# Performance work log

Measured on AMD Instinct MI355X. Metric: run time of the kernel, lower is better.

## Reference

```python
import jax, jax.numpy as jnp
import numpy as np

NUM_LONGTERM_MEM = 16  # config.num_longterm_mem


def setup_inputs() -> dict:
    key = jax.random.key(0)
    ks = jax.random.split(key, 9)
    B, T, C, H = 32, 2048, 768, 1536
    s = 0.02
    return {
        "x": jax.random.normal(ks[0], (B, T, C), jnp.float32),
        "Wq": jax.random.normal(ks[1], (C, C), jnp.float32) * s,
        "bq": jax.random.normal(ks[2], (C,), jnp.float32) * s,
        "W0": jax.random.normal(ks[3], (B, H, C), jnp.float32) * s,
        "b0": jax.random.normal(ks[4], (B, H), jnp.float32) * s,
        "W1": jax.random.normal(ks[5], (B, C, H), jnp.float32) * s,
        "b1": jax.random.normal(ks[6], (B, C), jnp.float32) * s,
        "Wo": jax.random.normal(ks[7], (C, C), jnp.float32) * s,
        "bo": jax.random.normal(ks[8], (C,), jnp.float32) * s,
    }


def reference(x, Wq, bq, W0, b0, W1, b1, Wo, bo):
    # x: [B, T, C]. Per-sample memory MLP weights W0 [B,H,C], W1 [B,C,H].
    B, T, C = x.shape
    L = NUM_LONGTERM_MEM
    # query projection (nn.Linear: x @ W^T + b)
    q = jnp.einsum("btc,dc->btd", x, Wq) + bq                       # [B,T,C]
    # per-sample 2-layer memory MLP with SiLU
    h = jax.nn.silu(jnp.einsum("btc,bhc->bth", q, W0) + b0[:, None, :])  # [B,T,H]
    mem = jnp.einsum("bth,bch->btc", h, W1) + b1[:, None, :]        # [B,T,C]
    # adaptive_avg_pool1d over T -> L (T divisible by L => uniform window mean)
    pooled = mem.reshape(B, L, T // L, C).mean(axis=2)              # [B,L,C]
    # output projection
    return jnp.einsum("blc,dc->bld", pooled, Wo) + bo               # [B,L,C]
```

## Files before the change

kernel.cpp:

```cpp
#include <hip/hip_runtime.h>
#include <stdint.h>

#define B_ 32
#define T_ 2048
#define C_ 768
#define H_ 1536
#define L_ 16

typedef unsigned short u16;
typedef __bf16 bf16x8 __attribute__((ext_vector_type(8)));
typedef float f32x4 __attribute__((ext_vector_type(4)));

__device__ __forceinline__ u16 f2bf(float f) {
    union { float f; uint32_t u; } v; v.f = f;
    uint32_t r = (v.u + 0x7fffu + ((v.u >> 16) & 1u)) >> 16;
    return (u16)r;
}

__device__ __forceinline__ float wave_sum(float v) {
    v += __shfl_xor(v, 1);  v += __shfl_xor(v, 2);  v += __shfl_xor(v, 4);
    v += __shfl_xor(v, 8);  v += __shfl_xor(v, 16); v += __shfl_xor(v, 32);
    return v;
}

__global__ void k_cvt(const float* __restrict__ in, u16* __restrict__ out, int n4) {
    int stride = gridDim.x * blockDim.x;
    for (int i = blockIdx.x * blockDim.x + threadIdx.x; i < n4; i += stride) {
        float4 v = reinterpret_cast<const float4*>(in)[i];
        ushort4 o;
        o.x = f2bf(v.x); o.y = f2bf(v.y); o.z = f2bf(v.z); o.w = f2bf(v.w);
        reinterpret_cast<ushort4*>(out)[i] = o;
    }
}

__global__ void k_prep1(const float* __restrict__ Wq, u16* __restrict__ WqTb,
                        const float* __restrict__ W0, u16* __restrict__ W0b,
                        const float* __restrict__ bq, const float* __restrict__ b0,
                        float* __restrict__ b0f, int e0) {
    const int t = threadIdx.x;
    if (blockIdx.x < (unsigned)e0) {
        const int w = t >> 6, lane = t & 63;
        const int nWaves = e0 * 4;
        const float4* bq4 = reinterpret_cast<const float4*>(bq);
        float4 b4_0 = bq4[lane], b4_1 = bq4[64 + lane], b4_2 = bq4[128 + lane];
        for (int rr = blockIdx.x * 4 + w; rr < B_ * H_; rr += nWaves) {
            const float4* src = reinterpret_cast<const float4*>(W0 + (size_t)rr * 768);
            ushort4* dst = reinterpret_cast<ushort4*>(W0b + (size_t)rr * 768);
            float4 v0 = src[lane], v1 = src[64 + lane], v2 = src[128 + lane];
            ushort4 o0, o1, o2;
            o0.x = f2bf(v0.x); o0.y = f2bf(v0.y); o0.z = f2bf(v0.z); o0.w = f2bf(v0.w);
            o1.x = f2bf(v1.x); o1.y = f2bf(v1.y); o1.z = f2bf(v1.z); o1.w = f2bf(v1.w);
            o2.x = f2bf(v2.x); o2.y = f2bf(v2.y); o2.z = f2bf(v2.z); o2.w = f2bf(v2.w);
            dst[lane] = o0; dst[64 + lane] = o1; dst[128 + lane] = o2;
            float dot = v0.x * b4_0.x + v0.y * b4_0.y + v0.z * b4_0.z + v0.w * b4_0.w
                      + v1.x * b4_1.x + v1.y * b4_1.y + v1.z * b4_1.z + v1.w * b4_1.w
                      + v2.x * b4_2.x + v2.y * b4_2.y + v2.z * b4_2.z + v2.w * b4_2.w;
            dot = wave_sum(dot);
            if (lane == 0) b0f[rr] = b0[rr] + dot;
        }
    } else {
        __shared__ u16 tl[64 * 65];
        const int nb = gridDim.x - e0;
        for (int tile = blockIdx.x - e0; tile < 144; tile += nb) {
            int d0 = (tile / 12) * 64, c0 = (tile % 12) * 64;
            __syncthreads();
#pragma unroll
            for (int p = 0; p < 16; ++p) {
                int idx = p * 256 + t;
                int r = idx >> 6, c = idx & 63;
                tl[r * 65 + c] = f2bf(Wq[(size_t)(d0 + r) * 768 + c0 + c]);
            }
            __syncthreads();
#pragma unroll
            for (int p = 0; p < 16; ++p) {
                int idx = p * 256 + t;
                int r = idx >> 6, c = idx & 63;
                WqTb[(size_t)(c0 + r) * 768 + d0 + c] = tl[c * 65 + r];
            }
        }
    }
}

__device__ __forceinline__ void gload16(const u16* g, u16* l) {
    __builtin_amdgcn_global_load_lds((const __attribute__((address_space(1))) void*)g,
                                     (__attribute__((address_space(3))) void*)l, 16, 0, 0);
}

template <int EPI>
__global__ __launch_bounds__(512, 2) void k_gemm9(const u16* __restrict__ Aall,
                                                  const u16* __restrict__ Ball,
                                                  const float* __restrict__ biasall,
                                                  u16* __restrict__ qout,
                                                  float* __restrict__ ph) {
    __shared__ u16 sm[81920];
    const int t = threadIdx.x;
    const int w = t >> 6, lane = t & 63;
    const int wr = w >> 2, wc = w & 3;
    const int l15 = lane & 15, kq = lane >> 4, cx = lane & 7;

    const int gx = gridDim.x, gy = gridDim.y;
    const int nwg = gx * gy * gridDim.z;
    int flat = blockIdx.x + gx * (blockIdx.y + gy * blockIdx.z);
    if ((nwg & 7) == 0) flat = (flat & 7) * (nwg >> 3) + (flat >> 3);
    const int bx = flat % gx;
    const int tmp = flat / gx;
    const int by = tmp % gy;
    const int bz = tmp / gy;

    const int n0 = bx * 256;
    const int m0 = by * 256;
    const u16* A; const u16* Bm; const float* bias;
    if constexpr (EPI == 0) {
        A = Aall + (size_t)m0 * C_;
        Bm = Ball + (size_t)n0 * C_;
        bias = biasall + n0;
    } else {
        A = Aall + ((size_t)bz * T_ + m0) * C_;
        Bm = Ball + ((size_t)bz * H_ + n0) * C_;
        bias = biasall + (size_t)bz * H_ + n0;
    }

    const int rl = (w << 4) + (lane >> 3);
    const int cs = (((lane & 7) ^ ((lane >> 3) & 7)) << 3);
    const int ldst = (w << 10);

    auto stA = [&](int kt, int buf) {
#pragma unroll
        for (int h = 0; h < 2; ++h) {
            const u16* g = A + (size_t)(h * 128 + rl) * C_ + kt * 64 + cs;
            u16* l = sm + buf * 16384 + h * 8192 + ldst;
            gload16(g, l);
            gload16(g + 8 * C_, l + 512);
        }
    };
    auto stB = [&](int kt, int buf) {
#pragma unroll
        for (int h = 0; h < 2; ++h) {
            const u16* g = Bm + (size_t)(h * 128 + rl) * C_ + kt * 64 + cs;
            u16* l = sm + 49152 + buf * 16384 + h * 8192 + ldst;
            gload16(g, l);
            gload16(g + 8 * C_, l + 512);
        }
    };

    f32x4 acc[8][4];
#pragma unroll
    for (int m = 0; m < 8; ++m)
#pragma unroll
        for (int n = 0; n < 4; ++n) acc[m][n] = (f32x4){0.f, 0.f, 0.f, 0.f};

    bf16x8 a0[4][2], a1[4][2], bfr[2][2];

    const int koff0 = ((kq ^ cx) << 3);
    const int koff1 = (((4 + kq) ^ cx) << 3);
    const u16* aB0 = sm + wr * 8192 + l15 * 64 + koff0;
    const u16* aB1 = sm + wr * 8192 + l15 * 64 + koff1;
    const u16* bB0 = sm + 49152 + (wc >> 1) * 8192 + (wc & 1) * 4096 + l15 * 64 + koff0;
    const u16* bB1 = sm + 49152 + (wc >> 1) * 8192 + (wc & 1) * 4096 + l15 * 64 + koff1;

    auto rdB0 = [&](int off) {
        bfr[0][0] = *reinterpret_cast<const bf16x8*>(bB0 + off);
        bfr[1][0] = *reinterpret_cast<const bf16x8*>(bB0 + off + 1024);
        bfr[0][1] = *reinterpret_cast<const bf16x8*>(bB1 + off);
        bfr[1][1] = *reinterpret_cast<const bf16x8*>(bB1 + off + 1024);
    };
    auto rdB1 = [&](int off) {
        bfr[0][0] = *reinterpret_cast<const bf16x8*>(bB0 + off + 2048);
        bfr[1][0] = *reinterpret_cast<const bf16x8*>(bB0 + off + 3072);
        bfr[0][1] = *reinterpret_cast<const bf16x8*>(bB1 + off + 2048);
        bfr[1][1] = *reinterpret_cast<const bf16x8*>(bB1 + off + 3072);
    };
    auto rdA0 = [&](int off) {
#pragma unroll
        for (int mm = 0; mm < 4; ++mm) {
            a0[mm][0] = *reinterpret_cast<const bf16x8*>(aB0 + off + mm * 1024);
            a0[mm][1] = *reinterpret_cast<const bf16x8*>(aB1 + off + mm * 1024);
        }
    };
    auto rdA1 = [&](int off) {
#pragma unroll
        for (int mm = 0; mm < 4; ++mm) {
            a1[mm][0] = *reinterpret_cast<const bf16x8*>(aB0 + off + 4096 + mm * 1024);
            a1[mm][1] = *reinterpret_cast<const bf16x8*>(aB1 + off + 4096 + mm * 1024);
        }
    };
    auto mma16 = [&](bf16x8 (&a)[4][2], int mq, int qn) {
        __builtin_amdgcn_s_setprio(1);
#pragma unroll
        for (int ks = 0; ks < 2; ++ks)
#pragma unroll
            for (int mm = 0; mm < 4; ++mm)
#pragma unroll
                for (int nn = 0; nn < 2; ++nn)
                    acc[mq * 4 + mm][qn * 2 + nn] = __builtin_amdgcn_mfma_f32_16x16x32_bf16(
                        a[mm][ks], bfr[nn][ks], acc[mq * 4 + mm][qn * 2 + nn], 0, 0, 0);
        __builtin_amdgcn_s_setprio(0);
    };

    stA(0, 0); stB(0, 0); stA(1, 1);
    asm volatile("s_waitcnt vmcnt(4)" ::: "memory");
    __builtin_amdgcn_s_barrier();

    int ba = 0;
#pragma unroll 1
    for (int kt = 0; kt < 12; ++kt) {
        const int bb = kt & 1;
        int ban = ba + 2; if (ban >= 3) ban -= 3;
        const bool s2 = (kt + 2 < 12);
        if (kt + 1 < 12) stB(kt + 1, bb ^ 1);
        if (s2) stA(kt + 2, ban);
        const int aoff = ba * 16384;
        const int boff = bb * 16384;
        rdB0(boff);
        rdA0(aoff);
        rdA1(aoff);
        mma16(a0, 0, 0);
        mma16(a1, 1, 0);
        __builtin_amdgcn_sched_barrier(0);
        rdB1(boff);
        mma16(a0, 0, 1);
        mma16(a1, 1, 1);
        if (s2) asm volatile("s_waitcnt vmcnt(4)" ::: "memory");
        else    asm volatile("s_waitcnt vmcnt(0)" ::: "memory");
        __builtin_amdgcn_s_barrier();
        ba = (ba + 1 == 3) ? 0 : ba + 1;
    }

    if constexpr (EPI == 0) {
        const int colb = n0 + wc * 64 + l15;
        const int rowb = m0 + wr * 128 + (kq << 2);
        float bv[4];
#pragma unroll
        for (int n = 0; n < 4; ++n) bv[n] = bias[wc * 64 + n * 16 + l15];
#pragma unroll
        for (int m = 0; m < 8; ++m)
#pragma unroll
            for (int r = 0; r < 4; ++r) {
                size_t ro = (size_t)(rowb + m * 16 + r) * C_;
#pragma unroll
                for (int n = 0; n < 4; ++n)
                    qout[ro + colb + n * 16] = f2bf(acc[m][n][r] + bv[n]);
            }
    } else {
        const int lwin = by * 2 + wr;
#pragma unroll
        for (int n = 0; n < 4; ++n) {
            int cloc = wc * 64 + n * 16 + l15;
            float bv = bias[cloc];
            float s = 0.f;
#pragma unroll
            for (int m = 0; m < 8; ++m)
#pragma unroll
                for (int r = 0; r < 4; ++r) {
                    float v = acc[m][n][r] + bv;
                    s += v / (1.f + __expf(-v));
                }
            s += __shfl_xor(s, 16);
            s += __shfl_xor(s, 32);
            if (kq == 0)
                ph[((size_t)bz * L_ + lwin) * H_ + n0 + cloc] = s * (1.f / 128.f);
        }
    }
}

__device__ __forceinline__ void stage_bf16_gload(const u16* gtile, int ld, u16* Ts,
                                                 int w, int lane) {
    const int r_in = lane >> 3;
    const int c0   = (lane & 7) << 3;
#pragma unroll
    for (int j = 0; j < 4; ++j) {
        int row = ((w << 2) + j) * 8 + r_in;
        const u16* g = gtile + (size_t)row * ld + c0;
        u16* l = Ts + (((w << 2) + j) << 9);
        gload16(g, l);
    }
}

__device__ __forceinline__ void mfma_tile(const u16* As, const u16* Bs,
                                          f32x4 (&acc)[4][4], int wr, int wc, int lane) {
#pragma unroll
    for (int ks = 0; ks < 2; ++ks) {
        const int ko = (ks << 5) + ((lane >> 4) << 3);
        bf16x8 a[4], b[4];
#pragma unroll
        for (int m = 0; m < 4; ++m)
            a[m] = *reinterpret_cast<const bf16x8*>(&As[(wr * 64 + m * 16 + (lane & 15)) * 64 + ko]);
#pragma unroll
        for (int n = 0; n < 4; ++n)
            b[n] = *reinterpret_cast<const bf16x8*>(&Bs[(wc * 64 + n * 16 + (lane & 15)) * 64 + ko]);
#pragma unroll
        for (int m = 0; m < 4; ++m)
#pragma unroll
            for (int n = 0; n < 4; ++n)
                acc[m][n] = __builtin_amdgcn_mfma_f32_16x16x32_bf16(a[m], b[n], acc[m][n], 0, 0, 0);
    }
}

__global__ __launch_bounds__(256, 2) void k_wf2(const u16* __restrict__ W0b,
                                                const u16* __restrict__ WqTb,
                                                u16* __restrict__ Wfb) {
    __shared__ u16 smw[128 * 136];
    u16* As = smw;
    u16* Bs = smw + 8192;
    const int t = threadIdx.x, w = t >> 6, lane = t & 63;
    const int wr = w >> 1, wc = w & 1;
    const int m0 = blockIdx.y * 128;
    const int n0 = blockIdx.x * 128;

    f32x4 acc[4][4];
#pragma unroll
    for (int m = 0; m < 4; ++m)
#pragma unroll
        for (int n = 0; n < 4; ++n) acc[m][n] = (f32x4){0.f, 0.f, 0.f, 0.f};

    for (int kt = 0; kt < 12; ++kt) {
        stage_bf16_gload(W0b + (size_t)m0 * C_ + kt * 64, C_, As, w, lane);
        stage_bf16_gload(WqTb + (size_t)n0 * C_ + kt * 64, C_, Bs, w, lane);
        __syncthreads();
        mfma_tile(As, Bs, acc, wr, wc, lane);
        __syncthreads();
    }

    const int lr0 = wr * 64 + ((lane >> 4) << 2);
    const int lc0 = wc * 64 + (lane & 15);
#pragma unroll
    for (int m = 0; m < 4; ++m)
#pragma unroll
        for (int n = 0; n < 4; ++n)
#pragma unroll
            for (int r = 0; r < 4; ++r)
                smw[(lr0 + m * 16 + r) * 136 + lc0 + n * 16] = f2bf(acc[m][n][r]);
    __syncthreads();
    u16* G = Wfb + (size_t)m0 * C_ + n0;
#pragma unroll
    for (int p = 0; p < 8; ++p) {
        int fl = p * 256 + t;
        int row = fl >> 4, c8 = fl & 15;
        f32x4 v = *reinterpret_cast<const f32x4*>(&smw[row * 136 + c8 * 8]);
        *reinterpret_cast<f32x4*>(&G[(size_t)row * C_ + c8 * 8]) = v;
    }
}

__global__ __launch_bounds__(256) void k_3a(const float* __restrict__ ph,
                                            const float* __restrict__ W1,
                                            const float* __restrict__ b1,
                                            float* __restrict__ pooled) {
    const int t = threadIdx.x, w = t >> 6, lane = t & 63;
    const int b  = blockIdx.y;
    const int cb = blockIdx.x * 16 + w * 4;

    float acc[4][16];
#pragma unroll
    for (int g = 0; g < 4; ++g)
#pragma unroll
        for (int l = 0; l < 16; ++l) acc[g][l] = 0.f;

    for (int i = 0; i < H_ / 256; ++i) {
        int h0 = i * 256 + lane * 4;
        float4 wv[4];
#pragma unroll
        for (int g = 0; g < 4; ++g)
            wv[g] = *reinterpret_cast<const float4*>(W1 + ((size_t)b * C_ + cb + g) * H_ + h0);
#pragma unroll
        for (int l = 0; l < 16; ++l) {
            float4 pv = *reinterpret_cast<const float4*>(ph + ((size_t)b * L_ + l) * H_ + h0);
#pragma unroll
            for (int g = 0; g < 4; ++g)
                acc[g][l] += wv[g].x * pv.x + wv[g].y * pv.y + wv[g].z * pv.z + wv[g].w * pv.w;
        }
    }
#pragma unroll
    for (int g = 0; g < 4; ++g)
#pragma unroll
        for (int l = 0; l < 16; ++l) acc[g][l] = wave_sum(acc[g][l]);

    if (lane < 16) {
#pragma unroll
        for (int g = 0; g < 4; ++g)
            pooled[((size_t)b * L_ + lane) * C_ + cb + g] = acc[g][lane] + b1[b * C_ + cb + g];
    }
}

__global__ __launch_bounds__(256) void k_3b(const float* __restrict__ pooled,
                                            const float* __restrict__ Wo,
                                            const float* __restrict__ bo,
                                            float* __restrict__ out) {
    __shared__ __align__(16) float ps[4 * 768];
    const int t = threadIdx.x, w = t >> 6, lane = t & 63;
    const int rr0 = blockIdx.x * 4;

    for (int idx = t; idx < 4 * 768; idx += 256)
        ps[idx] = pooled[(size_t)rr0 * 768 + idx];
    __syncthreads();

    for (int d = w; d < 768; d += 4) {
        float a0 = 0.f, a1 = 0.f, a2 = 0.f, a3 = 0.f;
#pragma unroll
        for (int i = 0; i < 3; ++i) {
            int c = i * 256 + lane * 4;
            float4 wv = *reinterpret_cast<const float4*>(Wo + (size_t)d * 768 + c);
            float4 p0 = *reinterpret_cast<const float4*>(&ps[0 * 768 + c]);
            float4 p1 = *reinterpret_cast<const float4*>(&ps[1 * 768 + c]);
            float4 p2 = *reinterpret_cast<const float4*>(&ps[2 * 768 + c]);
            float4 p3 = *reinterpret_cast<const float4*>(&ps[3 * 768 + c]);
            a0 += wv.x * p0.x + wv.y * p0.y + wv.z * p0.z + wv.w * p0.w;
            a1 += wv.x * p1.x + wv.y * p1.y + wv.z * p1.z + wv.w * p1.w;
            a2 += wv.x * p2.x + wv.y * p2.y + wv.z * p2.z + wv.w * p2.w;
            a3 += wv.x * p3.x + wv.y * p3.y + wv.z * p3.z + wv.w * p3.w;
        }
        a0 = wave_sum(a0); a1 = wave_sum(a1); a2 = wave_sum(a2); a3 = wave_sum(a3);
        if (lane == 0) {
            float bb = bo[d];
            out[(size_t)(rr0 + 0) * 768 + d] = a0 + bb;
            out[(size_t)(rr0 + 1) * 768 + d] = a1 + bb;
            out[(size_t)(rr0 + 2) * 768 + d] = a2 + bb;
            out[(size_t)(rr0 + 3) * 768 + d] = a3 + bb;
        }
    }
}

extern "C" void kernel_launch(void* const* d_in, const int* in_sizes, int n_in,
                              void* d_out, int out_size, void* d_ws, size_t ws_size,
                              hipStream_t stream) {
    const float* x  = (const float*)d_in[0];
    const float* Wq = (const float*)d_in[1];
    const float* bq = (const float*)d_in[2];
    const float* W0 = (const float*)d_in[3];
    const float* b0 = (const float*)d_in[4];
    const float* W1 = (const float*)d_in[5];
    const float* b1 = (const float*)d_in[6];
    const float* Wo = (const float*)d_in[7];
    const float* bo = (const float*)d_in[8];
    float* out = (float*)d_out;

    char* p = (char*)d_ws;
    size_t off = 0;
    auto carve = [&](size_t bytes) -> char* {
        char* r = p + off;
        off += (bytes + 255) & ~(size_t)255;
        return r;
    };
    float* ph     = (float*)carve((size_t)B_ * L_ * H_ * 4);
    float* pooled = (float*)carve((size_t)B_ * L_ * C_ * 4);

    const size_t xb_bytes  = (size_t)B_ * T_ * C_ * 2;
    const size_t w0b_bytes = (size_t)B_ * H_ * C_ * 2;
    const size_t wq_bytes  = (size_t)C_ * C_ * 2;
    const size_t b0f_bytes = (size_t)B_ * H_ * 4;

    const int n4x  = B_ * T_ * C_ / 4;
    const int n4wq = C_ * C_ / 4;
    const int n4w0 = B_ * H_ * C_ / 4;

    if (off + b0f_bytes + wq_bytes + w0b_bytes + xb_bytes + 1024 <= ws_size) {
        float* b0f  = (float*)carve(b0f_bytes);
        u16*   WqTb = (u16*)carve(wq_bytes);
        u16*   Wfb  = (u16*)carve(w0b_bytes);
        u16*   U    = (u16*)carve(xb_bytes);
        u16*   W0b  = U;
        u16*   xb   = U;

        k_prep1<<<dim3(2048), 256, 0, stream>>>(Wq, WqTb, W0, W0b, bq, b0, b0f, 2016);
        k_wf2<<<dim3(C_ / 128, (B_ * H_) / 128), 256, 0, stream>>>(W0b, WqTb, Wfb);
        k_cvt<<<dim3(2048), 256, 0, stream>>>(x, xb, n4x);
        k_gemm9<1><<<dim3(H_ / 256, T_ / 256, B_), 512, 0, stream>>>(xb, Wfb, b0f, nullptr, ph);
    } else {
        u16* qb  = (u16*)carve(xb_bytes);
        u16* Wqb = (u16*)carve(wq_bytes);
        u16* xb  = (u16*)carve(xb_bytes);
        u16* W0b = xb;
        k_cvt<<<dim3(64), 256, 0, stream>>>(Wq, Wqb, n4wq);
        k_cvt<<<dim3(2048), 256, 0, stream>>>(x, xb, n4x);
        k_gemm9<0><<<dim3(C_ / 256, (B_ * T_) / 256), 512, 0, stream>>>(xb, Wqb, bq, qb, nullptr);
        k_cvt<<<dim3(2048), 256, 0, stream>>>(W0, W0b, n4w0);
        k_gemm9<1><<<dim3(H_ / 256, T_ / 256, B_), 512, 0, stream>>>(qb, W0b, b0, nullptr, ph);
    }

    k_3a<<<dim3(C_ / 16, B_), 256, 0, stream>>>(ph, W1, b1, pooled);
    k_3b<<<dim3(B_ * L_ / 4), 256, 0, stream>>>(pooled, Wo, bo, out);
}
```

Baseline: 627.3 us.

## Fuse x conversion into prep kernel and convert W0 on the fly in Wf GEMM

Merges the x-to-bf16 conversion into the prep kernel as a third block partition, which removes one launch and lets that conversion overlap with the W0 bias-dot and Wq transpose work. The W0 bf16 copy is no longer written out. Instead the Wf GEMM loads fp32 W0 tiles directly and converts them to bf16 while staging into shared memory. This drops a full write and re-read of W0 in bf16, at the cost of reading fp32 in the GEMM through synchronous loads rather than direct global-to-LDS loads.

```diff
diff --git a/kernel.cpp b/kernel.cpp
--- a/kernel.cpp
+++ b/kernel.cpp
@@ -33,25 +33,28 @@
     }
 }
 
-__global__ void k_prep1(const float* __restrict__ Wq, u16* __restrict__ WqTb,
-                        const float* __restrict__ W0, u16* __restrict__ W0b,
-                        const float* __restrict__ bq, const float* __restrict__ b0,
-                        float* __restrict__ b0f, int e0) {
+__global__ void k_prep_all(const float* __restrict__ x, u16* __restrict__ xb, int n4x,
+                           const float* __restrict__ Wq, u16* __restrict__ WqTb,
+                           const float* __restrict__ W0,
+                           const float* __restrict__ bq, const float* __restrict__ b0,
+                           float* __restrict__ b0f, int e0, int e1) {
     const int t = threadIdx.x;
     if (blockIdx.x < (unsigned)e0) {
+        int stride = e0 * 256;
+        for (int i = blockIdx.x * 256 + t; i < n4x; i += stride) {
+            float4 v = reinterpret_cast<const float4*>(x)[i];
+            ushort4 o;
+            o.x = f2bf(v.x); o.y = f2bf(v.y); o.z = f2bf(v.z); o.w = f2bf(v.w);
+            reinterpret_cast<ushort4*>(xb)[i] = o;
+        }
+    } else if (blockIdx.x < (unsigned)e1) {
         const int w = t >> 6, lane = t & 63;
-        const int nWaves = e0 * 4;
+        const int nWaves = (e1 - e0) * 4;
         const float4* bq4 = reinterpret_cast<const float4*>(bq);
         float4 b4_0 = bq4[lane], b4_1 = bq4[64 + lane], b4_2 = bq4[128 + lane];
-        for (int rr = blockIdx.x * 4 + w; rr < B_ * H_; rr += nWaves) {
+        for (int rr = (blockIdx.x - e0) * 4 + w; rr < B_ * H_; rr += nWaves) {
             const float4* src = reinterpret_cast<const float4*>(W0 + (size_t)rr * 768);
-            ushort4* dst = reinterpret_cast<ushort4*>(W0b + (size_t)rr * 768);
             float4 v0 = src[lane], v1 = src[64 + lane], v2 = src[128 + lane];
-            ushort4 o0, o1, o2;
-            o0.x = f2bf(v0.x); o0.y = f2bf(v0.y); o0.z = f2bf(v0.z); o0.w = f2bf(v0.w);
-            o1.x = f2bf(v1.x); o1.y = f2bf(v1.y); o1.z = f2bf(v1.z); o1.w = f2bf(v1.w);
-            o2.x = f2bf(v2.x); o2.y = f2bf(v2.y); o2.z = f2bf(v2.z); o2.w = f2bf(v2.w);
-            dst[lane] = o0; dst[64 + lane] = o1; dst[128 + lane] = o2;
             float dot = v0.x * b4_0.x + v0.y * b4_0.y + v0.z * b4_0.z + v0.w * b4_0.w
                       + v1.x * b4_1.x + v1.y * b4_1.y + v1.z * b4_1.z + v1.w * b4_1.w
                       + v2.x * b4_2.x + v2.y * b4_2.y + v2.z * b4_2.z + v2.w * b4_2.w;
@@ -60,8 +63,8 @@
         }
     } else {
         __shared__ u16 tl[64 * 65];
-        const int nb = gridDim.x - e0;
-        for (int tile = blockIdx.x - e0; tile < 144; tile += nb) {
+        const int nb = gridDim.x - e1;
+        for (int tile = blockIdx.x - e1; tile < 144; tile += nb) {
             int d0 = (tile / 12) * 64, c0 = (tile % 12) * 64;
             __syncthreads();
 #pragma unroll
@@ -276,6 +279,19 @@
     }
 }
 
+__device__ __forceinline__ void stage_f32_cvt(const float* gtile, int ld, u16* Ts, int t) {
+#pragma unroll
+    for (int i = 0; i < 8; ++i) {
+        int slot = t + (i << 8);
+        int row  = slot >> 4;
+        int c4   = (slot & 15) << 2;
+        float4 v = *reinterpret_cast<const float4*>(gtile + (size_t)row * ld + c4);
+        ushort4 o;
+        o.x = f2bf(v.x); o.y = f2bf(v.y); o.z = f2bf(v.z); o.w = f2bf(v.w);
+        *reinterpret_cast<ushort4*>(&Ts[row * 64 + c4]) = o;
+    }
+}
+
 __device__ __forceinline__ void mfma_tile(const u16* As, const u16* Bs,
                                           f32x4 (&acc)[4][4], int wr, int wc, int lane) {
 #pragma unroll
@@ -296,7 +312,7 @@
     }
 }
 
-__global__ __launch_bounds__(256, 2) void k_wf2(const u16* __restrict__ W0b,
+__global__ __launch_bounds__(256, 2) void k_wf3(const float* __restrict__ W0,
                                                 const u16* __restrict__ WqTb,
                                                 u16* __restrict__ Wfb) {
     __shared__ u16 smw[128 * 136];
@@ -314,7 +330,7 @@
         for (int n = 0; n < 4; ++n) acc[m][n] = (f32x4){0.f, 0.f, 0.f, 0.f};
 
     for (int kt = 0; kt < 12; ++kt) {
-        stage_bf16_gload(W0b + (size_t)m0 * C_ + kt * 64, C_, As, w, lane);
+        stage_f32_cvt(W0 + (size_t)m0 * C_ + kt * 64, C_, As, t);
         stage_bf16_gload(WqTb + (size_t)n0 * C_ + kt * 64, C_, Bs, w, lane);
         __syncthreads();
         mfma_tile(As, Bs, acc, wr, wc, lane);
@@ -456,13 +472,11 @@
         float* b0f  = (float*)carve(b0f_bytes);
         u16*   WqTb = (u16*)carve(wq_bytes);
         u16*   Wfb  = (u16*)carve(w0b_bytes);
-        u16*   U    = (u16*)carve(xb_bytes);
-        u16*   W0b  = U;
-        u16*   xb   = U;
-
-        k_prep1<<<dim3(2048), 256, 0, stream>>>(Wq, WqTb, W0, W0b, bq, b0, b0f, 2016);
-        k_wf2<<<dim3(C_ / 128, (B_ * H_) / 128), 256, 0, stream>>>(W0b, WqTb, Wfb);
-        k_cvt<<<dim3(2048), 256, 0, stream>>>(x, xb, n4x);
+        u16*   xb   = (u16*)carve(xb_bytes);
+
+        k_prep_all<<<dim3(4096), 256, 0, stream>>>(x, xb, n4x, Wq, WqTb, W0,
+                                                   bq, b0, b0f, 2704, 4060);
+        k_wf3<<<dim3(C_ / 128, (B_ * H_) / 128), 256, 0, stream>>>(W0, WqTb, Wfb);
         k_gemm9<1><<<dim3(H_ / 256, T_ / 256, B_), 512, 0, stream>>>(xb, Wfb, b0f, nullptr, ph);
     } else {
         u16* qb  = (u16*)carve(xb_bytes);
```

Result: slower. 703.6 us (+12.2%).
